# Kernel tuning notes

Hardware: AMD Instinct MI355X
Metric: run time of the kernel (lower is better)

Reference implementation:

```python
import jax, jax.numpy as jnp
import numpy as np

# Model dims: H features, N half-state-size, R low-rank, CH output channels, KL kernel length
H, N, R, CH, KL = 512, 64, 1, 1, 4096


def setup_inputs() -> dict:
    key = jax.random.key(0)
    ks = jax.random.split(key, 8)
    log_dt = jax.random.uniform(ks[0], (H,), minval=float(np.log(1e-3)), maxval=float(np.log(1e-1)), dtype=jnp.float32)
    # Hurwitz-like poles: negative real part, HiPPO-like imaginary ladder
    w_re = -0.5 - jax.random.uniform(ks[1], (H, N), dtype=jnp.float32)
    w_im = jnp.broadcast_to(np.float32(np.pi) * jnp.arange(N, dtype=jnp.float32), (H, N))
    B_re = jax.random.normal(ks[2], (1, H, N), dtype=jnp.float32)
    B_im = jax.random.normal(ks[3], (1, H, N), dtype=jnp.float32)
    # small low-rank correction keeps the Woodbury denominator away from zero
    P_re = 0.1 * jax.random.normal(ks[4], (R, H, N), dtype=jnp.float32)
    P_im = 0.1 * jax.random.normal(ks[5], (R, H, N), dtype=jnp.float32)
    C_re = jax.random.normal(ks[6], (CH, H, N), dtype=jnp.float32)
    C_im = jax.random.normal(ks[7], (CH, H, N), dtype=jnp.float32)
    return dict(log_dt=log_dt, w_re=w_re, w_im=w_im, B_re=B_re, B_im=B_im,
                P_re=P_re, P_im=P_im, C_re=C_re, C_im=C_im, L=KL)


def _kernel(log_dt, w_re, w_im, B_re, B_im, P_re, P_im, C_re, C_im, L):
    dt = jnp.exp(log_dt)                                   # (H,)
    w = (w_re + 1j * w_im) * dt[:, None]                   # (H,N) discretized poles w*dt
    B = B_re + 1j * B_im                                   # (1,H,N)
    P = P_re + 1j * P_im                                   # (R,H,N)
    Q = jnp.conj(P)                                        # hurwitz=False path: Q = conj(P)
    C = C_re + 1j * C_im                                   # (CH,H,N)

    Lf = L // 2 + 1
    kk = jnp.arange(Lf)
    omega = jnp.exp((-2j * np.pi) * kk / L)                # FFT roots of unity (complex64)
    den = 1.0 + omega
    # Nyquist node (omega = -1) handled analytically below; guard the division
    safe_den = jnp.where(jnp.abs(den) < 1e-6, jnp.ones_like(den), den)
    z = 2.0 * (1.0 - omega) / safe_den                     # bilinear-transform nodes

    Bc = jnp.concatenate([B, P], axis=0)                   # (1+R,H,N)
    Cc = jnp.concatenate([C, Q], axis=0)                   # (CH+R,H,N)
    v = Bc[:, None] * Cc[None]                             # (1+R,CH+R,H,N)

    # Cauchy kernel: r[a,b,h,l] = sum_n v[a,b,h,n] / (z[l] - w[h,n])
    recip = 1.0 / (z[None, None, :] - w[:, :, None])       # (H,N,Lf)
    r = jnp.einsum('abhn,hnl->abhl', v, recip)             # (1+R,CH+R,H,Lf)
    r = r * dt[None, None, :, None]

    # rank-1 Woodbury correction
    k_f = r[:-1, :-1] - r[:-1, -1:] * r[-1:, :-1] / (1.0 + r[-1:, -1:])
    k_f = k_f * 2.0 / safe_den

    if L % 2 == 0:
        # analytic z -> inf limit at the Nyquist node: dt/2 * sum_n v00
        nyq = 0.5 * dt[None, None, :] * jnp.sum(v[:-1, :-1], axis=-1)  # (1,CH,H)
        k_f = k_f.at[..., -1].set(nyq)

    k = jnp.fft.irfft(k_f, n=L, axis=-1)[..., :L]          # (1,CH,H,L) real
    return k[-1]                                           # (CH,H,L)


def reference(log_dt, w_re, w_im, B_re, B_im, P_re, P_im, C_re, C_im, L):
    return _kernel(log_dt, w_re, w_im, B_re, B_im, P_re, P_im, C_re, C_im, L)
```

## Files before the change

### kernel.cpp

```cpp
#include <hip/hip_runtime.h>
#include <hip/hip_bf16.h>
#include <math.h>


#define HH   512
#define NN   64
#define LLEN 4096
#define MM   2048
#define NTHREADS 1024
#define ZPAD(i) ((i) + ((i) >> 4))

typedef float v2f __attribute__((ext_vector_type(2)));

__global__ __launch_bounds__(NTHREADS, 8) void ssknplr_kernel(
    const float* __restrict__ log_dt,
    const float* __restrict__ w_re, const float* __restrict__ w_im,
    const float* __restrict__ B_re, const float* __restrict__ B_im,
    const float* __restrict__ P_re, const float* __restrict__ P_im,
    const float* __restrict__ C_re, const float* __restrict__ C_im,
    float* __restrict__ out)
{
    __shared__ v2f    s_pp[NN][10];
    __shared__ float2 s_Z[ZPAD(MM) + 1];
    __shared__ float2 s_tw[MM];

    const int h   = blockIdx.x;
    const int tid = threadIdx.x;
    const float dt = expf(log_dt[h]);

    if (tid < NN) {
        const int n   = tid;
        const int idx = h * NN + n;
        const float wr = w_re[idx] * dt;
        const float wi = w_im[idx] * dt;
        const float Br = B_re[idx], Bi = B_im[idx];
        const float Pr = P_re[idx], Pi = P_im[idx];
        const float Cr = C_re[idx], Ci = C_im[idx];
        const float vals[10] = {
            -wi, -wr, wr * wr,
            dt * (Br * Cr - Bi * Ci),
            dt * (Br * Ci + Bi * Cr),
            dt * (Br * Pr + Bi * Pi),
            dt * (Bi * Pr - Br * Pi),
            dt * (Pr * Cr - Pi * Ci),
            dt * (Pr * Ci + Pi * Cr),
            dt * (Pr * Pr + Pi * Pi)
        };
        #pragma unroll
        for (int j = 0; j < 10; ++j) s_pp[n][j] = (v2f){vals[j], vals[j]};
    }
    for (int i = tid; i < MM - 1; i += NTHREADS) {
        const int v = i + 1;
        const int s = 31 - __clz(v);
        const int j = v - (1 << s);
        const float ang = (float)j * (3.14159265358979323846f / (float)(1 << s));
        float sj, cj;
        sincosf(ang, &sj, &cj);
        s_tw[i] = make_float2(cj, sj);
    }
    __syncthreads();

    const float pi_over_L = 3.14159265358979323846f / (float)LLEN;
    v2f tv;
    tv.x = tanf(pi_over_L * (float)tid);
    tv.y = tanf(pi_over_L * (float)(tid + MM / 2));
    const v2f t2v = tv + tv;

    v2f a00r = 0.f, a00i = 0.f, a01r = 0.f, a01i = 0.f;
    v2f a10r = 0.f, a10i = 0.f, a11r = 0.f, a11i = 0.f;

    for (int n = 0; n < NN; ++n) {
        const v2f mwi = s_pp[n][0];
        const v2f nr  = s_pp[n][1];
        const v2f wr2 = s_pp[n][2];
        const v2f dim = t2v + mwi;
        const v2f den = __builtin_elementwise_fma(dim, dim, wr2);
        v2f inv;
        inv.x = __builtin_amdgcn_rcpf(den.x);
        inv.y = __builtin_amdgcn_rcpf(den.y);
        const v2f ur = nr * inv;
        const v2f ui = -(dim * inv);
        const v2f v00r = s_pp[n][3], v00i = s_pp[n][4];
        const v2f v01r = s_pp[n][5], v01i = s_pp[n][6];
        const v2f v10r = s_pp[n][7], v10i = s_pp[n][8];
        const v2f v11  = s_pp[n][9];
        a00r = __builtin_elementwise_fma( v00r, ur, a00r);
        a00r = __builtin_elementwise_fma(-v00i, ui, a00r);
        a00i = __builtin_elementwise_fma( v00r, ui, a00i);
        a00i = __builtin_elementwise_fma( v00i, ur, a00i);
        a01r = __builtin_elementwise_fma( v01r, ur, a01r);
        a01r = __builtin_elementwise_fma(-v01i, ui, a01r);
        a01i = __builtin_elementwise_fma( v01r, ui, a01i);
        a01i = __builtin_elementwise_fma( v01i, ur, a01i);
        a10r = __builtin_elementwise_fma( v10r, ur, a10r);
        a10r = __builtin_elementwise_fma(-v10i, ui, a10r);
        a10i = __builtin_elementwise_fma( v10r, ui, a10i);
        a10i = __builtin_elementwise_fma( v10i, ur, a10i);
        a11r = __builtin_elementwise_fma( v11,  ur, a11r);
        a11i = __builtin_elementwise_fma( v11,  ui, a11i);
    }

    {
        const v2f dr = a11r + 1.0f;
        const v2f di = a11i;
        const v2f dd = __builtin_elementwise_fma(dr, dr, di * di);
        v2f dinv;
        dinv.x = __builtin_amdgcn_rcpf(dd.x);
        dinv.y = __builtin_amdgcn_rcpf(dd.y);
        const v2f numr = a01r * a10r - a01i * a10i;
        const v2f numi = a01r * a10i + a01i * a10r;
        const v2f cr = (numr * dr + numi * di) * dinv;
        const v2f ci = (numi * dr - numr * di) * dinv;
        const v2f Wr = a00r - cr;
        const v2f Wi = a00i - ci;
        const v2f Kr = __builtin_elementwise_fma(-tv, Wi, Wr);
        const v2f Ki = __builtin_elementwise_fma( tv, Wr, Wi);
        s_Z[ZPAD(tid)] = make_float2(Kr.x, (tid == 0) ? 0.0f : Ki.x);
        s_Z[ZPAD(tid + MM / 2)] = make_float2(Kr.y, Ki.y);
    }
    if (tid == 0) {
        float sr = 0.f;
        for (int n = 0; n < NN; ++n) sr += s_pp[n][3].x;
        s_Z[ZPAD(MM)] = make_float2(0.5f * sr, 0.0f);
    }
    __syncthreads();

    {
        const float ang0 = 3.14159265358979323846f / (float)MM;
        const int k = tid;
        if (k == 0) {
            const float a = s_Z[ZPAD(0)].x;
            const float b = s_Z[ZPAD(MM)].x;
            s_Z[ZPAD(0)] = make_float2(0.5f * (a + b), 0.5f * (a - b));
            const float2 km = s_Z[ZPAD(MM / 2)];
            s_Z[ZPAD(MM / 2)] = make_float2(km.x, -km.y);
        } else {
            const float2 Ka = s_Z[ZPAD(k)];
            const float2 Kb = s_Z[ZPAD(MM - k)];
            float sk, ck;
            sincosf((float)k * ang0, &sk, &ck);
            const float Pr = 0.5f * (Ka.x + Kb.x), Pi = 0.5f * (Ka.y - Kb.y);
            const float Dr = 0.5f * (Ka.x - Kb.x), Di = 0.5f * (Ka.y + Kb.y);
            const float al = sk * Dr + ck * Di;
            const float be = ck * Dr - sk * Di;
            s_Z[ZPAD(k)]      = make_float2(Pr - al, Pi + be);
            s_Z[ZPAD(MM - k)] = make_float2(Pr + al, be - Pi);
        }
    }
    __syncthreads();

    for (int s = 10; s >= 1; --s) {
        const int half = 1 << s;
        const int b  = tid;
        const int j  = b & (half - 1);
        const int i0 = ((b >> s) << (s + 1)) + j;
        const int i1 = i0 + half;
        const float2 w = s_tw[(half - 1) + j];
        const float2 u = s_Z[ZPAD(i0)];
        const float2 v = s_Z[ZPAD(i1)];
        s_Z[ZPAD(i0)] = make_float2(u.x + v.x, u.y + v.y);
        const float dx = u.x - v.x, dy = u.y - v.y;
        s_Z[ZPAD(i1)] = make_float2(dx * w.x - dy * w.y, dx * w.y + dy * w.x);
        __syncthreads();
    }
    {
        const int i0 = tid << 1, i1 = i0 | 1;
        const float2 u = s_Z[ZPAD(i0)];
        const float2 v = s_Z[ZPAD(i1)];
        s_Z[ZPAD(i0)] = make_float2(u.x + v.x, u.y + v.y);
        s_Z[ZPAD(i1)] = make_float2(u.x - v.x, u.y - v.y);
    }
    __syncthreads();

    const float scale = 1.0f / (float)MM;
    float2* o2 = (float2*)out + (size_t)h * MM;
    #pragma unroll
    for (int q = 0; q < 2; ++q) {
        const int m = tid + q * NTHREADS;
        const int r = (int)(__brev((unsigned)m) >> 21);
        const float2 z = s_Z[ZPAD(r)];
        o2[m] = make_float2(z.x * scale, z.y * scale);
    }
}

extern "C" void kernel_launch(void* const* d_in, const int* in_sizes, int n_in,
                              void* d_out, int out_size, void* d_ws, size_t ws_size,
                              hipStream_t stream) {
    const float* log_dt = (const float*)d_in[0];
    const float* w_re   = (const float*)d_in[1];
    const float* w_im   = (const float*)d_in[2];
    const float* B_re   = (const float*)d_in[3];
    const float* B_im   = (const float*)d_in[4];
    const float* P_re   = (const float*)d_in[5];
    const float* P_im   = (const float*)d_in[6];
    const float* C_re   = (const float*)d_in[7];
    const float* C_im   = (const float*)d_in[8];
    float* out = (float*)d_out;

    ssknplr_kernel<<<dim3(HH), dim3(NTHREADS), 0, stream>>>(
        log_dt, w_re, w_im, B_re, B_im, P_re, P_im, C_re, C_im, out);
}
```

Before: 39.59 us.

## Precompute per-pole coefficients in a separate kernel and read them from global memory

Moves the per-pole coefficient computation into a separate pole_kernel that writes to workspace. The main kernel then reads those coefficients straight from global memory (uniform loads) instead of staging them in shared memory behind a barrier. The goal is to remove the serialized prologue in which only 64 threads compute while the rest wait. In exchange it adds a second kernel launch and global reads inside the hot loop, relying on the cache. The old path is kept as a fallback when the workspace is too small.

After: 39.45 us. Within noise of the previous version (-0.4%).

```diff
diff --git a/kernel.cpp b/kernel.cpp
--- a/kernel.cpp
+++ b/kernel.cpp
@@ -12,42 +12,72 @@
 
 typedef float v2f __attribute__((ext_vector_type(2)));
 
+__device__ __forceinline__ void pole_vals(
+    float dt, float wr, float wi, float Br, float Bi,
+    float Pr, float Pi, float Cr, float Ci, float* vals)
+{
+    vals[0] = -wi;
+    vals[1] = -wr;
+    vals[2] = wr * wr;
+    vals[3] = dt * (Br * Cr - Bi * Ci);
+    vals[4] = dt * (Br * Ci + Bi * Cr);
+    vals[5] = dt * (Br * Pr + Bi * Pi);
+    vals[6] = dt * (Bi * Pr - Br * Pi);
+    vals[7] = dt * (Pr * Cr - Pi * Ci);
+    vals[8] = dt * (Pr * Ci + Pi * Cr);
+    vals[9] = dt * (Pr * Pr + Pi * Pi);
+}
+
+__global__ __launch_bounds__(256) void pole_kernel(
+    const float* __restrict__ log_dt,
+    const float* __restrict__ w_re, const float* __restrict__ w_im,
+    const float* __restrict__ B_re, const float* __restrict__ B_im,
+    const float* __restrict__ P_re, const float* __restrict__ P_im,
+    const float* __restrict__ C_re, const float* __restrict__ C_im,
+    v2f* __restrict__ pp)
+{
+    const int g = blockIdx.x * 256 + threadIdx.x;
+    const int h = g >> 6;
+    const float dt = expf(log_dt[h]);
+    const float wr = w_re[g] * dt, wi = w_im[g] * dt;
+    float vals[10];
+    pole_vals(dt, wr, wi, B_re[g], B_im[g], P_re[g], P_im[g], C_re[g], C_im[g], vals);
+    v2f* o = pp + (size_t)g * 10;
+    #pragma unroll
+    for (int j = 0; j < 10; ++j) o[j] = (v2f){vals[j], vals[j]};
+}
+
+template<bool GPP>
 __global__ __launch_bounds__(NTHREADS, 8) void ssknplr_kernel(
     const float* __restrict__ log_dt,
     const float* __restrict__ w_re, const float* __restrict__ w_im,
     const float* __restrict__ B_re, const float* __restrict__ B_im,
     const float* __restrict__ P_re, const float* __restrict__ P_im,
     const float* __restrict__ C_re, const float* __restrict__ C_im,
+    const v2f* __restrict__ pp,
     float* __restrict__ out)
 {
-    __shared__ v2f    s_pp[NN][10];
     __shared__ float2 s_Z[ZPAD(MM) + 1];
     __shared__ float2 s_tw[MM];
+    __shared__ v2f    s_pp[GPP ? 1 : NN * 10];
 
     const int h   = blockIdx.x;
     const int tid = threadIdx.x;
-    const float dt = expf(log_dt[h]);
-
-    if (tid < NN) {
-        const int n   = tid;
-        const int idx = h * NN + n;
-        const float wr = w_re[idx] * dt;
-        const float wi = w_im[idx] * dt;
-        const float Br = B_re[idx], Bi = B_im[idx];
-        const float Pr = P_re[idx], Pi = P_im[idx];
-        const float Cr = C_re[idx], Ci = C_im[idx];
-        const float vals[10] = {
-            -wi, -wr, wr * wr,
-            dt * (Br * Cr - Bi * Ci),
-            dt * (Br * Ci + Bi * Cr),
-            dt * (Br * Pr + Bi * Pi),
-            dt * (Bi * Pr - Br * Pi),
-            dt * (Pr * Cr - Pi * Ci),
-            dt * (Pr * Ci + Pi * Cr),
-            dt * (Pr * Pr + Pi * Pi)
-        };
-        #pragma unroll
-        for (int j = 0; j < 10; ++j) s_pp[n][j] = (v2f){vals[j], vals[j]};
+
+    const v2f* __restrict__ pg = pp + (size_t)h * (NN * 10);
+
+    if constexpr (!GPP) {
+        if (tid < NN) {
+            const int n   = tid;
+            const int idx = h * NN + n;
+            const float dt = expf(log_dt[h]);
+            const float wr = w_re[idx] * dt, wi = w_im[idx] * dt;
+            float vals[10];
+            pole_vals(dt, wr, wi, B_re[idx], B_im[idx], P_re[idx], P_im[idx],
+                      C_re[idx], C_im[idx], vals);
+            #pragma unroll
+            for (int j = 0; j < 10; ++j) s_pp[n * 10 + j] = (v2f){vals[j], vals[j]};
+        }
     }
     for (int i = tid; i < MM - 1; i += NTHREADS) {
         const int v = i + 1;
@@ -70,9 +100,20 @@
     v2f a10r = 0.f, a10i = 0.f, a11r = 0.f, a11i = 0.f;
 
     for (int n = 0; n < NN; ++n) {
-        const v2f mwi = s_pp[n][0];
-        const v2f nr  = s_pp[n][1];
-        const v2f wr2 = s_pp[n][2];
+        v2f mwi, nr, wr2, v00r, v00i, v01r, v01i, v10r, v10i, v11;
+        if constexpr (GPP) {
+            mwi  = pg[n * 10 + 0]; nr   = pg[n * 10 + 1]; wr2 = pg[n * 10 + 2];
+            v00r = pg[n * 10 + 3]; v00i = pg[n * 10 + 4];
+            v01r = pg[n * 10 + 5]; v01i = pg[n * 10 + 6];
+            v10r = pg[n * 10 + 7]; v10i = pg[n * 10 + 8];
+            v11  = pg[n * 10 + 9];
+        } else {
+            mwi  = s_pp[n * 10 + 0]; nr   = s_pp[n * 10 + 1]; wr2 = s_pp[n * 10 + 2];
+            v00r = s_pp[n * 10 + 3]; v00i = s_pp[n * 10 + 4];
+            v01r = s_pp[n * 10 + 5]; v01i = s_pp[n * 10 + 6];
+            v10r = s_pp[n * 10 + 7]; v10i = s_pp[n * 10 + 8];
+            v11  = s_pp[n * 10 + 9];
+        }
         const v2f dim = t2v + mwi;
         const v2f den = __builtin_elementwise_fma(dim, dim, wr2);
         v2f inv;
@@ -80,10 +121,6 @@
         inv.y = __builtin_amdgcn_rcpf(den.y);
         const v2f ur = nr * inv;
         const v2f ui = -(dim * inv);
-        const v2f v00r = s_pp[n][3], v00i = s_pp[n][4];
-        const v2f v01r = s_pp[n][5], v01i = s_pp[n][6];
-        const v2f v10r = s_pp[n][7], v10i = s_pp[n][8];
-        const v2f v11  = s_pp[n][9];
         a00r = __builtin_elementwise_fma( v00r, ur, a00r);
         a00r = __builtin_elementwise_fma(-v00i, ui, a00r);
         a00i = __builtin_elementwise_fma( v00r, ui, a00i);
@@ -120,7 +157,11 @@
     }
     if (tid == 0) {
         float sr = 0.f;
-        for (int n = 0; n < NN; ++n) sr += s_pp[n][3].x;
+        if constexpr (GPP) {
+            for (int n = 0; n < NN; ++n) sr += pg[n * 10 + 3].x;
+        } else {
+            for (int n = 0; n < NN; ++n) sr += s_pp[n * 10 + 3].x;
+        }
         s_Z[ZPAD(MM)] = make_float2(0.5f * sr, 0.0f);
     }
     __syncthreads();
@@ -197,6 +238,16 @@
     const float* C_im   = (const float*)d_in[8];
     float* out = (float*)d_out;
 
-    ssknplr_kernel<<<dim3(HH), dim3(NTHREADS), 0, stream>>>(
-        log_dt, w_re, w_im, B_re, B_im, P_re, P_im, C_re, C_im, out);
-}
+    const size_t pp_bytes = (size_t)HH * NN * 10 * sizeof(v2f);
+    if (ws_size >= pp_bytes) {
+        v2f* pp = (v2f*)d_ws;
+        pole_kernel<<<dim3(HH * NN / 256), dim3(256), 0, stream>>>(
+            log_dt, w_re, w_im, B_re, B_im, P_re, P_im, C_re, C_im, pp);
+        ssknplr_kernel<true><<<dim3(HH), dim3(NTHREADS), 0, stream>>>(
+            log_dt, w_re, w_im, B_re, B_im, P_re, P_im, C_re, C_im, pp, out);
+    } else {
+        ssknplr_kernel<false><<<dim3(HH), dim3(NTHREADS), 0, stream>>>(
+            log_dt, w_re, w_im, B_re, B_im, P_re, P_im, C_re, C_im,
+            (const v2f*)d_ws, out);
+    }
+}
```

## Use radix-4 FFT stages with on-the-fly hardware twiddles and shared reciprocal

Applied to the files above, without the earlier changes.

Replaces the radix-2 inverse FFT (10 stages, precomputed twiddle table) with five radix-4 stages whose twiddles are computed on the fly with hardware sin/cos intrinsics. This removes the shared twiddle table and its sincosf setup and halves the number of barriers. Also swaps tanf and sincosf for native amdgcn sin/cos/rcp, and computes the two Cauchy reciprocals from one rcp of their product. The radix-4 stages keep only half the threads busy, and the cheaper intrinsics plus the product-reciprocal trick may lose accuracy or overflow.

Result: faster. 38.09 us (-3.8%).

```diff
diff --git a/kernel.cpp b/kernel.cpp
--- a/kernel.cpp
+++ b/kernel.cpp
@@ -22,15 +22,14 @@
 {
     __shared__ v2f    s_pp[NN][10];
     __shared__ float2 s_Z[ZPAD(MM) + 1];
-    __shared__ float2 s_tw[MM];
 
     const int h   = blockIdx.x;
     const int tid = threadIdx.x;
-    const float dt = expf(log_dt[h]);
 
     if (tid < NN) {
         const int n   = tid;
         const int idx = h * NN + n;
+        const float dt = expf(log_dt[h]);
         const float wr = w_re[idx] * dt;
         const float wi = w_im[idx] * dt;
         const float Br = B_re[idx], Bi = B_im[idx];
@@ -49,35 +48,29 @@
         #pragma unroll
         for (int j = 0; j < 10; ++j) s_pp[n][j] = (v2f){vals[j], vals[j]};
     }
-    for (int i = tid; i < MM - 1; i += NTHREADS) {
-        const int v = i + 1;
-        const int s = 31 - __clz(v);
-        const int j = v - (1 << s);
-        const float ang = (float)j * (3.14159265358979323846f / (float)(1 << s));
-        float sj, cj;
-        sincosf(ang, &sj, &cj);
-        s_tw[i] = make_float2(cj, sj);
-    }
-    __syncthreads();
-
-    const float pi_over_L = 3.14159265358979323846f / (float)LLEN;
+    __syncthreads();
+
     v2f tv;
-    tv.x = tanf(pi_over_L * (float)tid);
-    tv.y = tanf(pi_over_L * (float)(tid + MM / 2));
+    {
+        const float rx = (float)tid * (1.0f / 8192.0f);
+        const float ry = (float)(tid + 1024) * (1.0f / 8192.0f);
+        tv.x = __builtin_amdgcn_sinf(rx) * __builtin_amdgcn_rcpf(__builtin_amdgcn_cosf(rx));
+        tv.y = __builtin_amdgcn_sinf(ry) * __builtin_amdgcn_rcpf(__builtin_amdgcn_cosf(ry));
+    }
     const v2f t2v = tv + tv;
 
     v2f a00r = 0.f, a00i = 0.f, a01r = 0.f, a01i = 0.f;
     v2f a10r = 0.f, a10i = 0.f, a11r = 0.f, a11i = 0.f;
 
     for (int n = 0; n < NN; ++n) {
-        const v2f mwi = s_pp[n][0];
-        const v2f nr  = s_pp[n][1];
-        const v2f wr2 = s_pp[n][2];
+        const v2f mwi  = s_pp[n][0];
+        const v2f nr   = s_pp[n][1];
+        const v2f wr2  = s_pp[n][2];
         const v2f dim = t2v + mwi;
         const v2f den = __builtin_elementwise_fma(dim, dim, wr2);
-        v2f inv;
-        inv.x = __builtin_amdgcn_rcpf(den.x);
-        inv.y = __builtin_amdgcn_rcpf(den.y);
+        const float ip = __builtin_amdgcn_rcpf(den.x * den.y);
+        const v2f dsw = __builtin_shufflevector(den, den, 1, 0);
+        const v2f inv = dsw * (v2f){ip, ip};
         const v2f ur = nr * inv;
         const v2f ui = -(dim * inv);
         const v2f v00r = s_pp[n][3], v00i = s_pp[n][4];
@@ -116,7 +109,7 @@
         const v2f Kr = __builtin_elementwise_fma(-tv, Wi, Wr);
         const v2f Ki = __builtin_elementwise_fma( tv, Wr, Wi);
         s_Z[ZPAD(tid)] = make_float2(Kr.x, (tid == 0) ? 0.0f : Ki.x);
-        s_Z[ZPAD(tid + MM / 2)] = make_float2(Kr.y, Ki.y);
+        s_Z[ZPAD(tid + 1024)] = make_float2(Kr.y, Ki.y);
     }
     if (tid == 0) {
         float sr = 0.f;
@@ -126,7 +119,6 @@
     __syncthreads();
 
     {
-        const float ang0 = 3.14159265358979323846f / (float)MM;
         const int k = tid;
         if (k == 0) {
             const float a = s_Z[ZPAD(0)].x;
@@ -137,8 +129,9 @@
         } else {
             const float2 Ka = s_Z[ZPAD(k)];
             const float2 Kb = s_Z[ZPAD(MM - k)];
-            float sk, ck;
-            sincosf((float)k * ang0, &sk, &ck);
+            const float rk = (float)k * (1.0f / 4096.0f);
+            const float sk = __builtin_amdgcn_sinf(rk);
+            const float ck = __builtin_amdgcn_cosf(rk);
             const float Pr = 0.5f * (Ka.x + Kb.x), Pi = 0.5f * (Ka.y - Kb.y);
             const float Dr = 0.5f * (Ka.x - Kb.x), Di = 0.5f * (Ka.y + Kb.y);
             const float al = sk * Dr + ck * Di;
@@ -149,18 +142,37 @@
     }
     __syncthreads();
 
-    for (int s = 10; s >= 1; --s) {
-        const int half = 1 << s;
-        const int b  = tid;
-        const int j  = b & (half - 1);
-        const int i0 = ((b >> s) << (s + 1)) + j;
-        const int i1 = i0 + half;
-        const float2 w = s_tw[(half - 1) + j];
-        const float2 u = s_Z[ZPAD(i0)];
-        const float2 v = s_Z[ZPAD(i1)];
-        s_Z[ZPAD(i0)] = make_float2(u.x + v.x, u.y + v.y);
-        const float dx = u.x - v.x, dy = u.y - v.y;
-        s_Z[ZPAD(i1)] = make_float2(dx * w.x - dy * w.y, dx * w.y + dy * w.x);
+    for (int s = 10; s >= 1; s -= 2) {
+        const int H = 1 << s;
+        const int Q = H >> 1;
+        const float scale = __builtin_amdgcn_rcpf((float)(2 * H));
+        if (tid < 512) {
+            const int b    = tid;
+            const int j    = b & (Q - 1);
+            const int base = ((b >> (s - 1)) << (s + 1)) + j;
+            const int i0 = base, i1 = base + Q, i2 = base + H, i3 = base + H + Q;
+            const float rev = (float)j * scale;
+            const float c  = __builtin_amdgcn_cosf(rev);
+            const float sn = __builtin_amdgcn_sinf(rev);
+            const float wbr = c * c - sn * sn;
+            const float wbi = 2.0f * c * sn;
+            const float2 u0 = s_Z[ZPAD(i0)];
+            const float2 u1 = s_Z[ZPAD(i1)];
+            const float2 u2 = s_Z[ZPAD(i2)];
+            const float2 u3 = s_Z[ZPAD(i3)];
+            const float a0r = u0.x + u2.x, a0i = u0.y + u2.y;
+            const float d0r = u0.x - u2.x, d0i = u0.y - u2.y;
+            const float a1r = u1.x + u3.x, a1i = u1.y + u3.y;
+            const float d1r = u1.x - u3.x, d1i = u1.y - u3.y;
+            const float e0r = d0r * c  - d0i * sn, e0i = d0r * sn + d0i * c;
+            const float e1r = -(d1r * sn) - d1i * c, e1i = d1r * c - d1i * sn;
+            s_Z[ZPAD(i0)] = make_float2(a0r + a1r, a0i + a1i);
+            const float t0r = a0r - a1r, t0i = a0i - a1i;
+            s_Z[ZPAD(i1)] = make_float2(t0r * wbr - t0i * wbi, t0r * wbi + t0i * wbr);
+            s_Z[ZPAD(i2)] = make_float2(e0r + e1r, e0i + e1i);
+            const float t1r = e0r - e1r, t1i = e0i - e1i;
+            s_Z[ZPAD(i3)] = make_float2(t1r * wbr - t1i * wbi, t1r * wbi + t1i * wbr);
+        }
         __syncthreads();
     }
     {
```
